# Performance work log

Hardware: AMD Instinct MI355X
Metric: run time of the kernel (lower is better)

## Reference

```python
import jax, jax.numpy as jnp
import numpy as np

SIGMA = 30.0
N, E = 50000, 1600000
IN_LOCAL, IN_GLOBAL, HIDDEN = 128, 128, 64


def setup_inputs() -> dict:
    key = jax.random.key(0)
    ks = jax.random.split(key, 20)
    inp = {}
    inp["x_local"] = jax.random.normal(ks[0], (N, IN_LOCAL), jnp.float32)
    inp["x_global"] = jax.random.normal(ks[1], (N, IN_GLOBAL), jnp.float32)
    inp["noise_features"] = jax.random.normal(ks[2], (N, 10), jnp.float32)
    inp["coord"] = jax.random.normal(ks[3], (N, 2), jnp.float32) * 30.0
    inp["edge_index"] = jax.random.randint(ks[4], (2, E), 0, N, jnp.int32)
    # EdgeWeightLayer params (torch init: eye fc1 weight, fixed fc2 weight, zero fc2 bias)
    inp["fc1_w"] = jnp.eye(10, dtype=jnp.float32)
    inp["fc1_b"] = jax.random.uniform(ks[5], (10,), jnp.float32, -0.3, 0.3)
    inp["fc2_w"] = jnp.array([[1.0, 0.7, 0.5, 0.3, -0.5, -0.8, -0.3, -0.5, 0.2, -0.2]], jnp.float32)
    inp["fc2_b"] = jnp.zeros((1,), jnp.float32)
    sl = 1.0 / np.sqrt(IN_LOCAL)
    inp["gat_w"] = jax.random.uniform(ks[6], (HIDDEN, IN_LOCAL), jnp.float32, -sl, sl)
    inp["gat_att_src"] = jax.random.uniform(ks[7], (HIDDEN,), jnp.float32, -sl, sl)
    inp["gat_att_dst"] = jax.random.uniform(ks[8], (HIDDEN,), jnp.float32, -sl, sl)
    inp["gat_b"] = jnp.zeros((HIDDEN,), jnp.float32)
    sg = 1.0 / np.sqrt(IN_GLOBAL)
    inp["gcn_w"] = jax.random.uniform(ks[9], (HIDDEN, IN_GLOBAL), jnp.float32, -sg, sg)
    inp["gcn_b"] = jnp.zeros((HIDDEN,), jnp.float32)
    sf = 1.0 / np.sqrt(2 * HIDDEN)
    inp["fus_w1"] = jax.random.uniform(ks[10], (HIDDEN, 2 * HIDDEN), jnp.float32, -sf, sf)
    inp["fus_b1"] = jax.random.uniform(ks[11], (HIDDEN,), jnp.float32, -sf, sf)
    sh = 1.0 / np.sqrt(HIDDEN)
    inp["fus_w2"] = jax.random.uniform(ks[12], (1, HIDDEN), jnp.float32, -sh, sh)
    inp["fus_b2"] = jax.random.uniform(ks[13], (1,), jnp.float32, -sh, sh)
    return inp


def _forward(edge_index, x_local, x_global, noise_features, coord,
             fc1_w, fc1_b, fc2_w, fc2_b,
             gat_w, gat_att_src, gat_att_dst, gat_b,
             gcn_w, gcn_b, fus_w1, fus_b1, fus_w2, fus_b2):
    n = x_local.shape[0]
    src, dst = edge_index[0], edge_index[1]

    # per-edge noise MLP on gathered source node features: [E,10]->[E]
    h = jax.nn.elu(noise_features[src] @ fc1_w.T + fc1_b)
    noise_ind = (h @ fc2_w.T + fc2_b)[:, 0]

    # gaussian distance kernel + smooth mapping into [0.1, 2.0]
    d2 = jnp.sum((coord[src] - coord[dst]) ** 2, axis=1)
    gw = jnp.exp(-d2 / (2.0 * SIGMA ** 2))
    w = 0.1 + 1.9 * jax.nn.sigmoid(gw * (1.0 + noise_ind) - 1.0)
    mask = w >= 0.2  # dynamic edge masking, expressed as weight masking (jit-safe)

    # append self loops (both GATConv and GCNConv add them by default)
    loop = jnp.arange(n, dtype=src.dtype)
    s_all = jnp.concatenate([src, loop])
    d_all = jnp.concatenate([dst, loop])
    m_all = jnp.concatenate([mask, jnp.ones((n,), bool)])

    # ---- GAT branch (1 head; PyG GATConv ignores scalar edge weight when edge_dim=None) ----
    xl = x_local @ gat_w.T                           # [N, H]
    a_src = xl @ gat_att_src                         # [N]
    a_dst = xl @ gat_att_dst
    e = jax.nn.leaky_relu(a_src[s_all] + a_dst[d_all], negative_slope=0.2)
    neg = jnp.finfo(e.dtype).min
    mx = jax.ops.segment_max(jnp.where(m_all, e, neg), d_all, num_segments=n)
    ex = jnp.where(m_all, jnp.exp(e - mx[d_all]), 0.0)
    den = jax.ops.segment_sum(ex, d_all, num_segments=n)
    alpha = ex / den[d_all]
    gat_out = jax.ops.segment_sum(alpha[:, None] * xl[s_all], d_all, num_segments=n) + gat_b
    x_l = jax.nn.elu(gat_out)

    # ---- GCN branch (symmetric norm with masked edge weights, self-loop weight 1) ----
    ew = jnp.concatenate([jnp.where(mask, w, 0.0), jnp.ones((n,), w.dtype)])
    deg = jax.ops.segment_sum(ew, d_all, num_segments=n)
    dis = jnp.where(deg > 0, jax.lax.rsqrt(deg), 0.0)
    norm = dis[s_all] * ew * dis[d_all]
    xg = x_global @ gcn_w.T                          # [N, H]
    gcn_out = jax.ops.segment_sum(norm[:, None] * xg[s_all], d_all, num_segments=n) + gcn_b
    x_g = jax.nn.relu(gcn_out)

    # ---- fusion head (dropout inactive at inference) ----
    cat = jnp.concatenate([x_l, x_g], axis=1)        # [N, 2H]
    hid = jax.nn.relu(cat @ fus_w1.T + fus_b1)
    out = hid @ fus_w2.T + fus_b2                    # [N, 1]
    return out[:, 0]


def reference(x_local, x_global, noise_features, coord, edge_index,
              fc1_w, fc1_b, fc2_w, fc2_b,
              gat_w, gat_att_src, gat_att_dst, gat_b,
              gcn_w, gcn_b, fus_w1, fus_b1, fus_w2, fus_b2):
    return _forward(edge_index, x_local, x_global, noise_features, coord,
                    fc1_w, fc1_b, fc2_w, fc2_b,
                    gat_w, gat_att_src, gat_att_dst, gat_b,
                    gcn_w, gcn_b, fus_w1, fus_b1, fus_w2, fus_b2)
```

## Files before the change

### kernel.cpp

```cpp
#include <hip/hip_runtime.h>
#include <hip/hip_fp16.h>
#include <math.h>

#define NN 50000
#define NE 1600000
#define NBIN 512
#define DSTF 98
#define NREP 8
#define PCAP 24
#define BCAPR 576

__device__ __forceinline__ float wave_sum(float v) {
    #pragma unroll
    for (int off = 32; off > 0; off >>= 1) v += __shfl_xor(v, off, 64);
    return v;
}

__global__ __launch_bounds__(256) void k_node_gat(
    const float* __restrict__ x_local, const float* __restrict__ gat_w,
    const float* __restrict__ att_src, const float* __restrict__ att_dst,
    const float* __restrict__ nf, const float* __restrict__ coord,
    const float* __restrict__ fc1_w, const float* __restrict__ fc1_b,
    const float* __restrict__ fc2_w, const float* __restrict__ fc2_b,
    __half* __restrict__ xch,
    float4* __restrict__ snode, float4* __restrict__ dnode,
    float* __restrict__ ps)
{
    __shared__ float wL[64 * 132];
    __shared__ float xt[32 * 128];
    for (int f = threadIdx.x; f < 64 * 128; f += 256) {
        int h = f >> 7, k = f & 127;
        wL[h * 132 + k] = gat_w[f];
    }
    const int lane = threadIdx.x & 63;
    const int wid  = threadIdx.x >> 6;
    const float asv = att_src[lane];
    const float adv = att_dst[lane];
    const float4* wrow = (const float4*)(wL + lane * 132);
    float4* xts = (float4*)xt;
    const float4* xp = (const float4*)x_local;
    for (int base = blockIdx.x * 32; base < NN; base += gridDim.x * 32) {
        __syncthreads();
        #pragma unroll
        for (int k = 0; k < 4; k++) {
            int gi = base * 32 + (int)threadIdx.x + k * 256;
            if (gi < NN * 32) xts[threadIdx.x + k * 256] = xp[gi];
        }
        __syncthreads();
        float acc[8] = {0.f,0.f,0.f,0.f,0.f,0.f,0.f,0.f};
        const float4* xrow = (const float4*)(xt + wid * 8 * 128);
        #pragma unroll 1
        for (int t = 0; t < 32; t++) {
            float4 wv = wrow[t];
            #pragma unroll
            for (int j = 0; j < 8; j++) {
                float4 xv = xrow[j * 32 + t];
                acc[j] = fmaf(xv.x, wv.x, acc[j]);
                acc[j] = fmaf(xv.y, wv.y, acc[j]);
                acc[j] = fmaf(xv.z, wv.z, acc[j]);
                acc[j] = fmaf(xv.w, wv.w, acc[j]);
            }
        }
        float sv[8], dv[8];
        #pragma unroll
        for (int j = 0; j < 8; j++) {
            int n = base + wid * 8 + j;
            if (n < NN) xch[(size_t)n * 128 + lane] = __float2half(acc[j]);
            sv[j] = wave_sum(acc[j] * asv);
            dv[j] = wave_sum(acc[j] * adv);
        }
        if (lane < 8) {
            int n = base + wid * 8 + lane;
            if (n < NN) {
                float svx = (lane==0)?sv[0]:(lane==1)?sv[1]:(lane==2)?sv[2]:(lane==3)?sv[3]
                           :(lane==4)?sv[4]:(lane==5)?sv[5]:(lane==6)?sv[6]:sv[7];
                float dvx = (lane==0)?dv[0]:(lane==1)?dv[1]:(lane==2)?dv[2]:(lane==3)?dv[3]
                           :(lane==4)?dv[4]:(lane==5)?dv[5]:(lane==6)?dv[6]:dv[7];
                float xvv[10];
                #pragma unroll
                for (int k = 0; k < 10; k++) xvv[k] = nf[n * 10 + k];
                float niv = fc2_b[0];
                #pragma unroll
                for (int j = 0; j < 10; j++) {
                    float h = fc1_b[j];
                    #pragma unroll
                    for (int k = 0; k < 10; k++) h = fmaf(xvv[k], fc1_w[j * 10 + k], h);
                    h = (h > 0.f) ? h : expm1f(h);
                    niv = fmaf(h, fc2_w[j], niv);
                }
                float cx = coord[2 * n], cy = coord[2 * n + 1];
                float es = svx + dvx;
                es = (es >= 0.f) ? es : 0.2f * es;
                snode[n] = make_float4(cx, cy, svx, niv);
                dnode[n] = make_float4(cx, cy, dvx, 0.f);
                ps[n] = __expf(es);
            }
        }
    }
}

__global__ __launch_bounds__(256) void k_node_gcn(
    const float* __restrict__ x_global, const float* __restrict__ gcn_w,
    __half* __restrict__ xch)
{
    __shared__ float wL[64 * 132];
    __shared__ float xt[32 * 128];
    for (int f = threadIdx.x; f < 64 * 128; f += 256) {
        int h = f >> 7, k = f & 127;
        wL[h * 132 + k] = gcn_w[f];
    }
    const int lane = threadIdx.x & 63;
    const int wid  = threadIdx.x >> 6;
    const float4* wrow = (const float4*)(wL + lane * 132);
    float4* xts = (float4*)xt;
    const float4* xp = (const float4*)x_global;
    for (int base = blockIdx.x * 32; base < NN; base += gridDim.x * 32) {
        __syncthreads();
        #pragma unroll
        for (int k = 0; k < 4; k++) {
            int gi = base * 32 + (int)threadIdx.x + k * 256;
            if (gi < NN * 32) xts[threadIdx.x + k * 256] = xp[gi];
        }
        __syncthreads();
        float acc[8] = {0.f,0.f,0.f,0.f,0.f,0.f,0.f,0.f};
        const float4* xrow = (const float4*)(xt + wid * 8 * 128);
        #pragma unroll 1
        for (int t = 0; t < 32; t++) {
            float4 wv = wrow[t];
            #pragma unroll
            for (int j = 0; j < 8; j++) {
                float4 xv = xrow[j * 32 + t];
                acc[j] = fmaf(xv.x, wv.x, acc[j]);
                acc[j] = fmaf(xv.y, wv.y, acc[j]);
                acc[j] = fmaf(xv.z, wv.z, acc[j]);
                acc[j] = fmaf(xv.w, wv.w, acc[j]);
            }
        }
        #pragma unroll
        for (int j = 0; j < 8; j++) {
            int n = base + wid * 8 + j;
            if (n < NN) xch[(size_t)n * 128 + 64 + lane] = __float2half(acc[j]);
        }
    }
}

__global__ __launch_bounds__(256) void k_zerog(unsigned int* __restrict__ gcnt)
{
    int i = blockIdx.x * 256 + threadIdx.x;
    if (i < NREP * NBIN) gcnt[i] = 0u;
}

__global__ __launch_bounds__(256) void k_part2(
    const int* __restrict__ ei,
    unsigned int* __restrict__ bucket, unsigned int* __restrict__ gcnt)
{
    __shared__ unsigned int lcnt[NBIN];
    __shared__ unsigned int lbase[NBIN];
    __shared__ unsigned int lbuf[NBIN][PCAP];
    const int rep = blockIdx.x & 7;
    for (int t = threadIdx.x; t < NBIN; t += 256) lcnt[t] = 0u;
    __syncthreads();
    const int base = blockIdx.x * 2048;
    #pragma unroll
    for (int k = 0; k < 8; k++) {
        int i = base + k * 256 + threadIdx.x;
        if (i < NE) {
            int d = ei[NE + i];
            int s = ei[i];
            int b = d / DSTF;
            unsigned int pk = (unsigned int)s | ((unsigned int)(d - b * DSTF) << 16);
            unsigned int slot = atomicAdd(&lcnt[b], 1u);
            if (slot < PCAP) {
                lbuf[b][slot] = pk;
            } else {
                unsigned int g = atomicAdd(&gcnt[rep * NBIN + b], 1u);
                if (g < BCAPR) bucket[(size_t)(rep * NBIN + b) * BCAPR + g] = pk;
            }
        }
    }
    __syncthreads();
    for (int t = threadIdx.x; t < NBIN; t += 256) {
        unsigned int n = lcnt[t];
        if (n > PCAP) n = PCAP;
        lcnt[t] = n;
        lbase[t] = n ? atomicAdd(&gcnt[rep * NBIN + t], n) : 0u;
    }
    __syncthreads();
    for (int t = threadIdx.x; t < NBIN; t += 256) {
        unsigned int n = lcnt[t];
        unsigned int gb = lbase[t];
        unsigned int* dst = bucket + (size_t)(rep * NBIN + t) * BCAPR;
        for (unsigned int e = 0; e < n; e++) {
            unsigned int g = gb + e;
            if (g < BCAPR) dst[g] = lbuf[t][e];
        }
    }
}

__global__ __launch_bounds__(512) void k_edge3(
    const unsigned int* __restrict__ bucket, const unsigned int* __restrict__ gcnt,
    const float4* __restrict__ snode, const float4* __restrict__ dnode,
    uint2* __restrict__ rec, unsigned int* __restrict__ offA,
    unsigned int* __restrict__ cntA, float* __restrict__ dis)
{
    const int bin = blockIdx.x;
    const int d0  = bin * DSTF;
    __shared__ unsigned int cnt[DSTF], off[DSTF], cur[DSTF], ews[DSTF];
    __shared__ float4 dnd[DSTF];
    __shared__ unsigned int segc[NREP];
    __shared__ unsigned int sm[128];
    __shared__ unsigned int wsum[8];
    __shared__ unsigned int sbase;
    for (int t = threadIdx.x; t < DSTF; t += 512) {
        cnt[t] = 0u; cur[t] = 0u; ews[t] = 0u;
        int d = d0 + t;
        dnd[t] = (d < NN) ? dnode[d] : make_float4(0.f, 0.f, 0.f, 0.f);
    }
    if (threadIdx.x < NREP) {
        unsigned int c = gcnt[threadIdx.x * NBIN + bin];
        segc[threadIdx.x] = (c > BCAPR) ? BCAPR : c;
    }
    unsigned int partial = 0u;
    for (int idx = threadIdx.x; idx < NREP * NBIN; idx += 512) {
        int b = idx & (NBIN - 1);
        if (b < bin) {
            unsigned int c = gcnt[(idx >> 9) * NBIN + b];
            partial += (c > BCAPR) ? BCAPR : c;
        }
    }
    #pragma unroll
    for (int o = 32; o > 0; o >>= 1) partial += __shfl_xor(partial, o, 64);
    if ((threadIdx.x & 63) == 0) wsum[threadIdx.x >> 6] = partial;
    __syncthreads();
    if (threadIdx.x == 0) {
        unsigned int a = 0;
        #pragma unroll
        for (int r = 0; r < 8; r++) a += wsum[r];
        sbase = a;
    }
    __syncthreads();
    #pragma unroll
    for (int r = 0; r < NREP; r++) {
        unsigned int c = segc[r];
        const unsigned int* bk = bucket + (size_t)(r * NBIN + bin) * BCAPR;
        for (unsigned int t = threadIdx.x; t < c; t += 512)
            atomicAdd(&cnt[bk[t] >> 16], 1u);
    }
    __syncthreads();
    if (threadIdx.x < 128) sm[threadIdx.x] = (threadIdx.x < DSTF) ? cnt[threadIdx.x] : 0u;
    __syncthreads();
    for (int o = 1; o < 128; o <<= 1) {
        unsigned int t = 0;
        if (threadIdx.x < 128 && threadIdx.x >= o) t = sm[threadIdx.x - o];
        __syncthreads();
        if (threadIdx.x < 128) sm[threadIdx.x] += t;
        __syncthreads();
    }
    if (threadIdx.x < DSTF) off[threadIdx.x] = sbase + sm[threadIdx.x] - cnt[threadIdx.x];
    __syncthreads();
    #pragma unroll
    for (int r = 0; r < NREP; r++) {
        unsigned int c = segc[r];
        const unsigned int* bk = bucket + (size_t)(r * NBIN + bin) * BCAPR;
        for (unsigned int t = threadIdx.x; t < c; t += 512) {
            unsigned int pk = bk[t];
            int dl = (int)(pk >> 16);
            int s  = (int)(pk & 0xFFFFu);
            float4 sv = snode[s];
            float4 dv = dnd[dl];
            float dx = sv.x - dv.x, dy = sv.y - dv.y;
            float gw = __expf((dx * dx + dy * dy) * (-1.0f / 1800.0f));
            float tt = fmaf(gw, 1.0f + sv.w, -1.0f);
            float sg = 1.0f / (1.0f + __expf(-tt));
            float w  = fmaf(1.9f, sg, 0.1f);
            float e  = sv.z + dv.z;
            e = (e >= 0.f) ? e : 0.2f * e;
            float ewv = (w >= 0.2f) ? w : 0.0f;
            float p = (ewv != 0.f) ? __expf(e) : 0.0f;
            unsigned int rk = atomicAdd(&cur[dl], 1u);
            atomicAdd(&ews[dl], (unsigned int)(ewv * 16777216.0f + 0.5f));
            __half2 h = __floats2half2_rn(p, ewv);
            rec[off[dl] + rk] = make_uint2((unsigned int)s, *(unsigned int*)&h);
        }
    }
    __syncthreads();
    for (int t = threadIdx.x; t < DSTF; t += 512) {
        int d = d0 + t;
        if (d < NN) {
            offA[d] = off[t];
            cntA[d] = cnt[t];
            dis[d]  = rsqrtf(1.0f + (float)ews[t] * (1.0f / 16777216.0f));
        }
    }
}

__global__ __launch_bounds__(256) void k_gather3(
    const __half* __restrict__ xch,
    const float* __restrict__ ps, const float* __restrict__ dis,
    const unsigned int* __restrict__ offA, const unsigned int* __restrict__ cntA,
    const uint2* __restrict__ rec,
    const float* __restrict__ gat_b, const float* __restrict__ gcn_b,
    uint2* __restrict__ catLh, uint2* __restrict__ catGh)
{
    const int lane = threadIdx.x & 63;
    const int wid  = threadIdx.x >> 6;
    const int eg   = lane >> 3;
    const int q    = lane & 7;
    const int fi   = q * 8;
    const float g0 = (eg == 0) ? 1.0f : 0.0f;
    const float4 gb0 = *(const float4*)(gat_b + fi);
    const float4 gb1 = *(const float4*)(gat_b + fi + 4);
    const float4 cb0 = *(const float4*)(gcn_b + fi);
    const float4 cb1 = *(const float4*)(gcn_b + fi + 4);
    for (int n = blockIdx.x * 4 + wid; n < NN; n += gridDim.x * 4) {
        float psv = ps[n] * g0;
        float dd = dis[n];
        int beg = (int)offA[n];
        int end = beg + (int)cntA[n];
        const uint4* rowd = (const uint4*)(xch + (size_t)n * 128);
        uint4 us = rowd[q];
        uint4 ug = rowd[q + 8];
        float2 d0 = __half22float2(*(const __half2*)&us.x);
        float2 d1 = __half22float2(*(const __half2*)&us.y);
        float2 d2 = __half22float2(*(const __half2*)&us.z);
        float2 d3 = __half22float2(*(const __half2*)&us.w);
        float2 e0 = __half22float2(*(const __half2*)&ug.x);
        float2 e1 = __half22float2(*(const __half2*)&ug.y);
        float2 e2 = __half22float2(*(const __half2*)&ug.z);
        float2 e3 = __half22float2(*(const __half2*)&ug.w);
        float aL[8], aC[8];
        aL[0] = psv * d0.x; aL[1] = psv * d0.y; aL[2] = psv * d1.x; aL[3] = psv * d1.y;
        aL[4] = psv * d2.x; aL[5] = psv * d2.y; aL[6] = psv * d3.x; aL[7] = psv * d3.y;
        float sw = dd * g0;
        aC[0] = sw * e0.x; aC[1] = sw * e0.y; aC[2] = sw * e1.x; aC[3] = sw * e1.y;
        aC[4] = sw * e2.x; aC[5] = sw * e2.y; aC[6] = sw * e3.x; aC[7] = sw * e3.y;
        float den = psv;
        int j = beg + eg;
        for (; j + 8 < end; j += 16) {
            uint2 r0 = rec[j];
            uint2 r1 = rec[j + 8];
            int s0 = (int)r0.x;
            int s1 = (int)r1.x;
            float2 pc0 = __half22float2(*(const __half2*)&r0.y);
            float2 pc1 = __half22float2(*(const __half2*)&r1.y);
            float c0 = dis[s0] * pc0.y;
            float c1 = dis[s1] * pc1.y;
            const uint4* row0 = (const uint4*)(xch + (size_t)s0 * 128);
            const uint4* row1 = (const uint4*)(xch + (size_t)s1 * 128);
            uint4 l0 = row0[q];
            uint4 g0v = row0[q + 8];
            uint4 l1 = row1[q];
            uint4 g1v = row1[q + 8];
            float2 t0, t1, t2, t3;
            t0 = __half22float2(*(const __half2*)&l0.x);
            t1 = __half22float2(*(const __half2*)&l0.y);
            t2 = __half22float2(*(const __half2*)&l0.z);
            t3 = __half22float2(*(const __half2*)&l0.w);
            aL[0] = fmaf(pc0.x, t0.x, aL[0]); aL[1] = fmaf(pc0.x, t0.y, aL[1]);
            aL[2] = fmaf(pc0.x, t1.x, aL[2]); aL[3] = fmaf(pc0.x, t1.y, aL[3]);
            aL[4] = fmaf(pc0.x, t2.x, aL[4]); aL[5] = fmaf(pc0.x, t2.y, aL[5]);
            aL[6] = fmaf(pc0.x, t3.x, aL[6]); aL[7] = fmaf(pc0.x, t3.y, aL[7]);
            t0 = __half22float2(*(const __half2*)&g0v.x);
            t1 = __half22float2(*(const __half2*)&g0v.y);
            t2 = __half22float2(*(const __half2*)&g0v.z);
            t3 = __half22float2(*(const __half2*)&g0v.w);
            aC[0] = fmaf(c0, t0.x, aC[0]); aC[1] = fmaf(c0, t0.y, aC[1]);
            aC[2] = fmaf(c0, t1.x, aC[2]); aC[3] = fmaf(c0, t1.y, aC[3]);
            aC[4] = fmaf(c0, t2.x, aC[4]); aC[5] = fmaf(c0, t2.y, aC[5]);
            aC[6] = fmaf(c0, t3.x, aC[6]); aC[7] = fmaf(c0, t3.y, aC[7]);
            t0 = __half22float2(*(const __half2*)&l1.x);
            t1 = __half22float2(*(const __half2*)&l1.y);
            t2 = __half22float2(*(const __half2*)&l1.z);
            t3 = __half22float2(*(const __half2*)&l1.w);
            aL[0] = fmaf(pc1.x, t0.x, aL[0]); aL[1] = fmaf(pc1.x, t0.y, aL[1]);
            aL[2] = fmaf(pc1.x, t1.x, aL[2]); aL[3] = fmaf(pc1.x, t1.y, aL[3]);
            aL[4] = fmaf(pc1.x, t2.x, aL[4]); aL[5] = fmaf(pc1.x, t2.y, aL[5]);
            aL[6] = fmaf(pc1.x, t3.x, aL[6]); aL[7] = fmaf(pc1.x, t3.y, aL[7]);
            t0 = __half22float2(*(const __half2*)&g1v.x);
            t1 = __half22float2(*(const __half2*)&g1v.y);
            t2 = __half22float2(*(const __half2*)&g1v.z);
            t3 = __half22float2(*(const __half2*)&g1v.w);
            aC[0] = fmaf(c1, t0.x, aC[0]); aC[1] = fmaf(c1, t0.y, aC[1]);
            aC[2] = fmaf(c1, t1.x, aC[2]); aC[3] = fmaf(c1, t1.y, aC[3]);
            aC[4] = fmaf(c1, t2.x, aC[4]); aC[5] = fmaf(c1, t2.y, aC[5]);
            aC[6] = fmaf(c1, t3.x, aC[6]); aC[7] = fmaf(c1, t3.y, aC[7]);
            den += pc0.x + pc1.x;
        }
        if (j < end) {
            uint2 r0 = rec[j];
            int s0 = (int)r0.x;
            float2 pc0 = __half22float2(*(const __half2*)&r0.y);
            float c0 = dis[s0] * pc0.y;
            const uint4* row0 = (const uint4*)(xch + (size_t)s0 * 128);
            uint4 l0 = row0[q];
            uint4 g0v = row0[q + 8];
            float2 t0, t1, t2, t3;
            t0 = __half22float2(*(const __half2*)&l0.x);
            t1 = __half22float2(*(const __half2*)&l0.y);
            t2 = __half22float2(*(const __half2*)&l0.z);
            t3 = __half22float2(*(const __half2*)&l0.w);
            aL[0] = fmaf(pc0.x, t0.x, aL[0]); aL[1] = fmaf(pc0.x, t0.y, aL[1]);
            aL[2] = fmaf(pc0.x, t1.x, aL[2]); aL[3] = fmaf(pc0.x, t1.y, aL[3]);
            aL[4] = fmaf(pc0.x, t2.x, aL[4]); aL[5] = fmaf(pc0.x, t2.y, aL[5]);
            aL[6] = fmaf(pc0.x, t3.x, aL[6]); aL[7] = fmaf(pc0.x, t3.y, aL[7]);
            t0 = __half22float2(*(const __half2*)&g0v.x);
            t1 = __half22float2(*(const __half2*)&g0v.y);
            t2 = __half22float2(*(const __half2*)&g0v.z);
            t3 = __half22float2(*(const __half2*)&g0v.w);
            aC[0] = fmaf(c0, t0.x, aC[0]); aC[1] = fmaf(c0, t0.y, aC[1]);
            aC[2] = fmaf(c0, t1.x, aC[2]); aC[3] = fmaf(c0, t1.y, aC[3]);
            aC[4] = fmaf(c0, t2.x, aC[4]); aC[5] = fmaf(c0, t2.y, aC[5]);
            aC[6] = fmaf(c0, t3.x, aC[6]); aC[7] = fmaf(c0, t3.y, aC[7]);
            den += pc0.x;
        }
        #pragma unroll
        for (int m = 8; m <= 32; m <<= 1) {
            #pragma unroll
            for (int k = 0; k < 8; k++) {
                aL[k] += __shfl_xor(aL[k], m, 64);
                aC[k] += __shfl_xor(aC[k], m, 64);
            }
            den += __shfl_xor(den, m, 64);
        }
        if (eg == 0) {
            float rd = 1.0f / den;
            float la[8], ga[8];
            la[0] = fmaf(aL[0], rd, gb0.x); la[1] = fmaf(aL[1], rd, gb0.y);
            la[2] = fmaf(aL[2], rd, gb0.z); la[3] = fmaf(aL[3], rd, gb0.w);
            la[4] = fmaf(aL[4], rd, gb1.x); la[5] = fmaf(aL[5], rd, gb1.y);
            la[6] = fmaf(aL[6], rd, gb1.z); la[7] = fmaf(aL[7], rd, gb1.w);
            ga[0] = fmaxf(fmaf(dd, aC[0], cb0.x), 0.f);
            ga[1] = fmaxf(fmaf(dd, aC[1], cb0.y), 0.f);
            ga[2] = fmaxf(fmaf(dd, aC[2], cb0.z), 0.f);
            ga[3] = fmaxf(fmaf(dd, aC[3], cb0.w), 0.f);
            ga[4] = fmaxf(fmaf(dd, aC[4], cb1.x), 0.f);
            ga[5] = fmaxf(fmaf(dd, aC[5], cb1.y), 0.f);
            ga[6] = fmaxf(fmaf(dd, aC[6], cb1.z), 0.f);
            ga[7] = fmaxf(fmaf(dd, aC[7], cb1.w), 0.f);
            #pragma unroll
            for (int k = 0; k < 8; k++)
                la[k] = (la[k] > 0.f) ? la[k] : expm1f(la[k]);
            __half2 l01 = __floats2half2_rn(la[0], la[1]);
            __half2 l23 = __floats2half2_rn(la[2], la[3]);
            __half2 l45 = __floats2half2_rn(la[4], la[5]);
            __half2 l67 = __floats2half2_rn(la[6], la[7]);
            __half2 g01 = __floats2half2_rn(ga[0], ga[1]);
            __half2 g23 = __floats2half2_rn(ga[2], ga[3]);
            __half2 g45 = __floats2half2_rn(ga[4], ga[5]);
            __half2 g67 = __floats2half2_rn(ga[6], ga[7]);
            catLh[(size_t)n * 16 + q * 2] =
                make_uint2(*(unsigned int*)&l01, *(unsigned int*)&l23);
            catLh[(size_t)n * 16 + q * 2 + 1] =
                make_uint2(*(unsigned int*)&l45, *(unsigned int*)&l67);
            catGh[(size_t)n * 16 + q * 2] =
                make_uint2(*(unsigned int*)&g01, *(unsigned int*)&g23);
            catGh[(size_t)n * 16 + q * 2 + 1] =
                make_uint2(*(unsigned int*)&g45, *(unsigned int*)&g67);
        }
    }
}

__global__ __launch_bounds__(256) void k_fuse(
    const uint2* __restrict__ catLh, const uint2* __restrict__ catGh,
    const float* __restrict__ fus_w1, const float* __restrict__ fus_b1,
    const float* __restrict__ fus_w2, const float* __restrict__ fus_b2,
    float* __restrict__ out)
{
    __shared__ float wS[64 * 132];
    __shared__ uint2 catS[32 * 33];
    const int nb = blockIdx.x * 32;
    for (int f = threadIdx.x; f < 64 * 128; f += 256) {
        int r = f >> 7, c = f & 127;
        wS[r * 132 + c] = fus_w1[f];
    }
    for (int f = threadIdx.x; f < 32 * 32; f += 256) {
        int i = f >> 5, c = f & 31;
        int n = nb + i;
        uint2 v = make_uint2(0u, 0u);
        if (n < NN) v = (c < 16) ? catLh[(size_t)n * 16 + c]
                                 : catGh[(size_t)n * 16 + (c - 16)];
        catS[i * 33 + c] = v;
    }
    __syncthreads();
    const int p = threadIdx.x >> 3;
    const int q = threadIdx.x & 7;
    const int n = nb + p;
    float hid[8];
    #pragma unroll
    for (int j = 0; j < 8; j++) {
        int jj = (q + j) & 7;
        hid[j] = fus_b1[q * 8 + jj];
    }
    const uint2* cp = catS + p * 33;
    #pragma unroll 2
    for (int kb = 0; kb < 32; kb++) {
        uint2 u = cp[kb];
        float2 a = __half22float2(*(const __half2*)&u.x);
        float2 b = __half22float2(*(const __half2*)&u.y);
        #pragma unroll
        for (int j = 0; j < 8; j++) {
            int jj = (q + j) & 7;
            float4 wv = *(const float4*)(wS + (size_t)(q * 8 + jj) * 132 + kb * 4);
            hid[j] = fmaf(wv.x, a.x, hid[j]);
            hid[j] = fmaf(wv.y, a.y, hid[j]);
            hid[j] = fmaf(wv.z, b.x, hid[j]);
            hid[j] = fmaf(wv.w, b.y, hid[j]);
        }
    }
    float acc = 0.f;
    #pragma unroll
    for (int j = 0; j < 8; j++) {
        int jj = (q + j) & 7;
        acc = fmaf(fmaxf(hid[j], 0.f), fus_w2[q * 8 + jj], acc);
    }
    acc += __shfl_xor(acc, 1, 64);
    acc += __shfl_xor(acc, 2, 64);
    acc += __shfl_xor(acc, 4, 64);
    if (q == 0 && n < NN) out[n] = acc + fus_b2[0];
}

extern "C" void kernel_launch(void* const* d_in, const int* in_sizes, int n_in,
                              void* d_out, int out_size, void* d_ws, size_t ws_size,
                              hipStream_t stream)
{
    const float* x_local  = (const float*)d_in[0];
    const float* x_global = (const float*)d_in[1];
    const float* nf       = (const float*)d_in[2];
    const float* coord    = (const float*)d_in[3];
    const int*   ei       = (const int*)d_in[4];
    const float* fc1_w    = (const float*)d_in[5];
    const float* fc1_b    = (const float*)d_in[6];
    const float* fc2_w    = (const float*)d_in[7];
    const float* fc2_b    = (const float*)d_in[8];
    const float* gat_w    = (const float*)d_in[9];
    const float* att_src  = (const float*)d_in[10];
    const float* att_dst  = (const float*)d_in[11];
    const float* gat_b    = (const float*)d_in[12];
    const float* gcn_w    = (const float*)d_in[13];
    const float* gcn_b    = (const float*)d_in[14];
    const float* fus_w1   = (const float*)d_in[15];
    const float* fus_b1   = (const float*)d_in[16];
    const float* fus_w2   = (const float*)d_in[17];
    const float* fus_b2   = (const float*)d_in[18];
    float* out = (float*)d_out;

    char* ws = (char*)d_ws;
    uint2*  rec  = (uint2*) (ws);
    __half* xch  = (__half*)(ws + 12800000);
    uint2*  catLh= (uint2*) (ws + 25600000);
    uint2*  catGh= (uint2*) (ws + 32000000);
    unsigned int* bucket = (unsigned int*)(ws + 25600000);
    float4* snode= (float4*)(ws + 38400000);
    float4* dnode= (float4*)(ws + 39200000);
    unsigned int* offA = (unsigned int*)(ws + 40000000);
    unsigned int* cntA = (unsigned int*)(ws + 40200000);
    float*  dis  = (float*) (ws + 40400000);
    float*  ps   = (float*) (ws + 40600000);
    unsigned int* gcnt = (unsigned int*)(ws + 40800000);
    (void)in_sizes; (void)n_in; (void)out_size; (void)ws_size;

    k_zerog<<<(NREP * NBIN + 255) / 256, 256, 0, stream>>>(gcnt);
    k_part2<<<782, 256, 0, stream>>>(ei, bucket, gcnt);
    k_node_gat<<<782, 256, 0, stream>>>(x_local, gat_w, att_src, att_dst,
                                        nf, coord, fc1_w, fc1_b, fc2_w, fc2_b,
                                        xch, snode, dnode, ps);
    k_node_gcn<<<782, 256, 0, stream>>>(x_global, gcn_w, xch);
    k_edge3<<<NBIN, 512, 0, stream>>>(bucket, gcnt, snode, dnode,
                                      rec, offA, cntA, dis);
    k_gather3<<<3125, 256, 0, stream>>>(xch, ps, dis, offA, cntA, rec,
                                        gat_b, gcn_b, catLh, catGh);
    k_fuse<<<(NN + 31) / 32, 256, 0, stream>>>(catLh, catGh,
                                               fus_w1, fus_b1, fus_w2, fus_b2, out);
}
```

Measured before the change: 323.0 us.

## Merge edge partition and both node projection kernels into one launch

Combines the edge bucketing kernel and the GAT and GCN node projection kernels into a single kernel whose blocks are split by block index into three roles. Each role keeps its original logic and reuses one shared-memory buffer sized for the largest role. The goal is to remove two kernel launches and the idle tail between them, letting the independent stages run concurrently on the GPU. In exchange every block reserves the largest shared-memory footprint, which can lower occupancy for the projection blocks.

```diff
diff --git a/kernel.cpp b/kernel.cpp
--- a/kernel.cpp
+++ b/kernel.cpp
@@ -9,6 +9,7 @@
 #define NREP 8
 #define PCAP 24
 #define BCAPR 576
+#define NBF 782
 
 __device__ __forceinline__ float wave_sum(float v) {
     #pragma unroll
@@ -16,183 +17,150 @@
     return v;
 }
 
-__global__ __launch_bounds__(256) void k_node_gat(
+__global__ __launch_bounds__(256) void k_zerog(unsigned int* __restrict__ gcnt)
+{
+    int i = blockIdx.x * 256 + threadIdx.x;
+    if (i < NREP * NBIN) gcnt[i] = 0u;
+}
+
+__global__ __launch_bounds__(256) void k_front(
+    const int* __restrict__ ei,
+    unsigned int* __restrict__ bucket, unsigned int* __restrict__ gcnt,
     const float* __restrict__ x_local, const float* __restrict__ gat_w,
     const float* __restrict__ att_src, const float* __restrict__ att_dst,
     const float* __restrict__ nf, const float* __restrict__ coord,
     const float* __restrict__ fc1_w, const float* __restrict__ fc1_b,
     const float* __restrict__ fc2_w, const float* __restrict__ fc2_b,
+    const float* __restrict__ x_global, const float* __restrict__ gcn_w,
     __half* __restrict__ xch,
     float4* __restrict__ snode, float4* __restrict__ dnode,
     float* __restrict__ ps)
 {
-    __shared__ float wL[64 * 132];
-    __shared__ float xt[32 * 128];
-    for (int f = threadIdx.x; f < 64 * 128; f += 256) {
-        int h = f >> 7, k = f & 127;
-        wL[h * 132 + k] = gat_w[f];
-    }
-    const int lane = threadIdx.x & 63;
-    const int wid  = threadIdx.x >> 6;
-    const float asv = att_src[lane];
-    const float adv = att_dst[lane];
-    const float4* wrow = (const float4*)(wL + lane * 132);
-    float4* xts = (float4*)xt;
-    const float4* xp = (const float4*)x_local;
-    for (int base = blockIdx.x * 32; base < NN; base += gridDim.x * 32) {
+    __shared__ unsigned int smem[13312];
+    const int bid = blockIdx.x;
+    if (bid < NBF) {
+        unsigned int* lcnt  = smem;
+        unsigned int* lbase = smem + NBIN;
+        unsigned int (*lbuf)[PCAP] = (unsigned int(*)[PCAP])(smem + 2 * NBIN);
+        const int rep = bid & 7;
+        for (int t = threadIdx.x; t < NBIN; t += 256) lcnt[t] = 0u;
         __syncthreads();
+        const int base = bid * 2048;
         #pragma unroll
-        for (int k = 0; k < 4; k++) {
-            int gi = base * 32 + (int)threadIdx.x + k * 256;
-            if (gi < NN * 32) xts[threadIdx.x + k * 256] = xp[gi];
+        for (int k = 0; k < 8; k++) {
+            int i = base + k * 256 + threadIdx.x;
+            if (i < NE) {
+                int d = ei[NE + i];
+                int s = ei[i];
+                int b = d / DSTF;
+                unsigned int pk = (unsigned int)s | ((unsigned int)(d - b * DSTF) << 16);
+                unsigned int slot = atomicAdd(&lcnt[b], 1u);
+                if (slot < PCAP) {
+                    lbuf[b][slot] = pk;
+                } else {
+                    unsigned int g = atomicAdd(&gcnt[rep * NBIN + b], 1u);
+                    if (g < BCAPR) bucket[(size_t)(rep * NBIN + b) * BCAPR + g] = pk;
+                }
+            }
         }
         __syncthreads();
-        float acc[8] = {0.f,0.f,0.f,0.f,0.f,0.f,0.f,0.f};
-        const float4* xrow = (const float4*)(xt + wid * 8 * 128);
-        #pragma unroll 1
-        for (int t = 0; t < 32; t++) {
-            float4 wv = wrow[t];
+        for (int t = threadIdx.x; t < NBIN; t += 256) {
+            unsigned int n = lcnt[t];
+            if (n > PCAP) n = PCAP;
+            lcnt[t] = n;
+            lbase[t] = n ? atomicAdd(&gcnt[rep * NBIN + t], n) : 0u;
+        }
+        __syncthreads();
+        for (int t = threadIdx.x; t < NBIN; t += 256) {
+            unsigned int n = lcnt[t];
+            unsigned int gb = lbase[t];
+            unsigned int* dst = bucket + (size_t)(rep * NBIN + t) * BCAPR;
+            for (unsigned int e = 0; e < n; e++) {
+                unsigned int g = gb + e;
+                if (g < BCAPR) dst[g] = lbuf[t][e];
+            }
+        }
+    } else {
+        const bool isGat = bid < 2 * NBF;
+        const int vb = isGat ? bid - NBF : bid - 2 * NBF;
+        const float* xsrc = isGat ? x_local : x_global;
+        const float* wsrc = isGat ? gat_w : gcn_w;
+        float* wL = (float*)smem;
+        float* xt = (float*)smem + 64 * 132;
+        for (int f = threadIdx.x; f < 64 * 128; f += 256) {
+            int h = f >> 7, k = f & 127;
+            wL[h * 132 + k] = wsrc[f];
+        }
+        const int lane = threadIdx.x & 63;
+        const int wid  = threadIdx.x >> 6;
+        const float asv = att_src[lane];
+        const float adv = att_dst[lane];
+        const int ofs = isGat ? 0 : 64;
+        const float4* wrow = (const float4*)(wL + lane * 132);
+        float4* xts = (float4*)xt;
+        const float4* xp = (const float4*)xsrc;
+        for (int base = vb * 32; base < NN; base += NBF * 32) {
+            __syncthreads();
+            #pragma unroll
+            for (int k = 0; k < 4; k++) {
+                int gi = base * 32 + (int)threadIdx.x + k * 256;
+                if (gi < NN * 32) xts[threadIdx.x + k * 256] = xp[gi];
+            }
+            __syncthreads();
+            float acc[8] = {0.f,0.f,0.f,0.f,0.f,0.f,0.f,0.f};
+            const float4* xrow = (const float4*)(xt + wid * 8 * 128);
+            #pragma unroll 1
+            for (int t = 0; t < 32; t++) {
+                float4 wv = wrow[t];
+                #pragma unroll
+                for (int j = 0; j < 8; j++) {
+                    float4 xv = xrow[j * 32 + t];
+                    acc[j] = fmaf(xv.x, wv.x, acc[j]);
+                    acc[j] = fmaf(xv.y, wv.y, acc[j]);
+                    acc[j] = fmaf(xv.z, wv.z, acc[j]);
+                    acc[j] = fmaf(xv.w, wv.w, acc[j]);
+                }
+            }
             #pragma unroll
             for (int j = 0; j < 8; j++) {
-                float4 xv = xrow[j * 32 + t];
-                acc[j] = fmaf(xv.x, wv.x, acc[j]);
-                acc[j] = fmaf(xv.y, wv.y, acc[j]);
-                acc[j] = fmaf(xv.z, wv.z, acc[j]);
-                acc[j] = fmaf(xv.w, wv.w, acc[j]);
-            }
-        }
-        float sv[8], dv[8];
-        #pragma unroll
-        for (int j = 0; j < 8; j++) {
-            int n = base + wid * 8 + j;
-            if (n < NN) xch[(size_t)n * 128 + lane] = __float2half(acc[j]);
-            sv[j] = wave_sum(acc[j] * asv);
-            dv[j] = wave_sum(acc[j] * adv);
-        }
-        if (lane < 8) {
-            int n = base + wid * 8 + lane;
-            if (n < NN) {
-                float svx = (lane==0)?sv[0]:(lane==1)?sv[1]:(lane==2)?sv[2]:(lane==3)?sv[3]
-                           :(lane==4)?sv[4]:(lane==5)?sv[5]:(lane==6)?sv[6]:sv[7];
-                float dvx = (lane==0)?dv[0]:(lane==1)?dv[1]:(lane==2)?dv[2]:(lane==3)?dv[3]
-                           :(lane==4)?dv[4]:(lane==5)?dv[5]:(lane==6)?dv[6]:dv[7];
-                float xvv[10];
+                int n = base + wid * 8 + j;
+                if (n < NN) xch[(size_t)n * 128 + ofs + lane] = __float2half(acc[j]);
+            }
+            if (isGat) {
+                float sv[8], dv[8];
                 #pragma unroll
-                for (int k = 0; k < 10; k++) xvv[k] = nf[n * 10 + k];
-                float niv = fc2_b[0];
-                #pragma unroll
-                for (int j = 0; j < 10; j++) {
-                    float h = fc1_b[j];
-                    #pragma unroll
-                    for (int k = 0; k < 10; k++) h = fmaf(xvv[k], fc1_w[j * 10 + k], h);
-                    h = (h > 0.f) ? h : expm1f(h);
-                    niv = fmaf(h, fc2_w[j], niv);
+                for (int j = 0; j < 8; j++) {
+                    sv[j] = wave_sum(acc[j] * asv);
+                    dv[j] = wave_sum(acc[j] * adv);
                 }
-                float cx = coord[2 * n], cy = coord[2 * n + 1];
-                float es = svx + dvx;
-                es = (es >= 0.f) ? es : 0.2f * es;
-                snode[n] = make_float4(cx, cy, svx, niv);
-                dnode[n] = make_float4(cx, cy, dvx, 0.f);
-                ps[n] = __expf(es);
-            }
-        }
-    }
-}
-
-__global__ __launch_bounds__(256) void k_node_gcn(
-    const float* __restrict__ x_global, const float* __restrict__ gcn_w,
-    __half* __restrict__ xch)
-{
-    __shared__ float wL[64 * 132];
-    __shared__ float xt[32 * 128];
-    for (int f = threadIdx.x; f < 64 * 128; f += 256) {
-        int h = f >> 7, k = f & 127;
-        wL[h * 132 + k] = gcn_w[f];
-    }
-    const int lane = threadIdx.x & 63;
-    const int wid  = threadIdx.x >> 6;
-    const float4* wrow = (const float4*)(wL + lane * 132);
-    float4* xts = (float4*)xt;
-    const float4* xp = (const float4*)x_global;
-    for (int base = blockIdx.x * 32; base < NN; base += gridDim.x * 32) {
-        __syncthreads();
-        #pragma unroll
-        for (int k = 0; k < 4; k++) {
-            int gi = base * 32 + (int)threadIdx.x + k * 256;
-            if (gi < NN * 32) xts[threadIdx.x + k * 256] = xp[gi];
-        }
-        __syncthreads();
-        float acc[8] = {0.f,0.f,0.f,0.f,0.f,0.f,0.f,0.f};
-        const float4* xrow = (const float4*)(xt + wid * 8 * 128);
-        #pragma unroll 1
-        for (int t = 0; t < 32; t++) {
-            float4 wv = wrow[t];
-            #pragma unroll
-            for (int j = 0; j < 8; j++) {
-                float4 xv = xrow[j * 32 + t];
-                acc[j] = fmaf(xv.x, wv.x, acc[j]);
-                acc[j] = fmaf(xv.y, wv.y, acc[j]);
-                acc[j] = fmaf(xv.z, wv.z, acc[j]);
-                acc[j] = fmaf(xv.w, wv.w, acc[j]);
-            }
-        }
-        #pragma unroll
-        for (int j = 0; j < 8; j++) {
-            int n = base + wid * 8 + j;
-            if (n < NN) xch[(size_t)n * 128 + 64 + lane] = __float2half(acc[j]);
-        }
-    }
-}
-
-__global__ __launch_bounds__(256) void k_zerog(unsigned int* __restrict__ gcnt)
-{
-    int i = blockIdx.x * 256 + threadIdx.x;
-    if (i < NREP * NBIN) gcnt[i] = 0u;
-}
-
-__global__ __launch_bounds__(256) void k_part2(
-    const int* __restrict__ ei,
-    unsigned int* __restrict__ bucket, unsigned int* __restrict__ gcnt)
-{
-    __shared__ unsigned int lcnt[NBIN];
-    __shared__ unsigned int lbase[NBIN];
-    __shared__ unsigned int lbuf[NBIN][PCAP];
-    const int rep = blockIdx.x & 7;
-    for (int t = threadIdx.x; t < NBIN; t += 256) lcnt[t] = 0u;
-    __syncthreads();
-    const int base = blockIdx.x * 2048;
-    #pragma unroll
-    for (int k = 0; k < 8; k++) {
-        int i = base + k * 256 + threadIdx.x;
-        if (i < NE) {
-            int d = ei[NE + i];
-            int s = ei[i];
-            int b = d / DSTF;
-            unsigned int pk = (unsigned int)s | ((unsigned int)(d - b * DSTF) << 16);
-            unsigned int slot = atomicAdd(&lcnt[b], 1u);
-            if (slot < PCAP) {
-                lbuf[b][slot] = pk;
-            } else {
-                unsigned int g = atomicAdd(&gcnt[rep * NBIN + b], 1u);
-                if (g < BCAPR) bucket[(size_t)(rep * NBIN + b) * BCAPR + g] = pk;
-            }
-        }
-    }
-    __syncthreads();
-    for (int t = threadIdx.x; t < NBIN; t += 256) {
-        unsigned int n = lcnt[t];
-        if (n > PCAP) n = PCAP;
-        lcnt[t] = n;
-        lbase[t] = n ? atomicAdd(&gcnt[rep * NBIN + t], n) : 0u;
-    }
-    __syncthreads();
-    for (int t = threadIdx.x; t < NBIN; t += 256) {
-        unsigned int n = lcnt[t];
-        unsigned int gb = lbase[t];
-        unsigned int* dst = bucket + (size_t)(rep * NBIN + t) * BCAPR;
-        for (unsigned int e = 0; e < n; e++) {
-            unsigned int g = gb + e;
-            if (g < BCAPR) dst[g] = lbuf[t][e];
+                if (lane < 8) {
+                    int n = base + wid * 8 + lane;
+                    if (n < NN) {
+                        float svx = (lane==0)?sv[0]:(lane==1)?sv[1]:(lane==2)?sv[2]:(lane==3)?sv[3]
+                                   :(lane==4)?sv[4]:(lane==5)?sv[5]:(lane==6)?sv[6]:sv[7];
+                        float dvx = (lane==0)?dv[0]:(lane==1)?dv[1]:(lane==2)?dv[2]:(lane==3)?dv[3]
+                                   :(lane==4)?dv[4]:(lane==5)?dv[5]:(lane==6)?dv[6]:dv[7];
+                        float xvv[10];
+                        #pragma unroll
+                        for (int k = 0; k < 10; k++) xvv[k] = nf[n * 10 + k];
+                        float niv = fc2_b[0];
+                        #pragma unroll
+                        for (int j = 0; j < 10; j++) {
+                            float h = fc1_b[j];
+                            #pragma unroll
+                            for (int k = 0; k < 10; k++) h = fmaf(xvv[k], fc1_w[j * 10 + k], h);
+                            h = (h > 0.f) ? h : expm1f(h);
+                            niv = fmaf(h, fc2_w[j], niv);
+                        }
+                        float cx = coord[2 * n], cy = coord[2 * n + 1];
+                        float es = svx + dvx;
+                        es = (es >= 0.f) ? es : 0.2f * es;
+                        snode[n] = make_float4(cx, cy, svx, niv);
+                        dnode[n] = make_float4(cx, cy, dvx, 0.f);
+                        ps[n] = __expf(es);
+                    }
+                }
+            }
         }
     }
 }
@@ -560,11 +528,11 @@
     (void)in_sizes; (void)n_in; (void)out_size; (void)ws_size;
 
     k_zerog<<<(NREP * NBIN + 255) / 256, 256, 0, stream>>>(gcnt);
-    k_part2<<<782, 256, 0, stream>>>(ei, bucket, gcnt);
-    k_node_gat<<<782, 256, 0, stream>>>(x_local, gat_w, att_src, att_dst,
-                                        nf, coord, fc1_w, fc1_b, fc2_w, fc2_b,
-                                        xch, snode, dnode, ps);
-    k_node_gcn<<<782, 256, 0, stream>>>(x_global, gcn_w, xch);
+    k_front<<<3 * NBF, 256, 0, stream>>>(ei, bucket, gcnt,
+                                         x_local, gat_w, att_src, att_dst,
+                                         nf, coord, fc1_w, fc1_b, fc2_w, fc2_b,
+                                         x_global, gcn_w,
+                                         xch, snode, dnode, ps);
     k_edge3<<<NBIN, 512, 0, stream>>>(bucket, gcnt, snode, dnode,
                                       rec, offA, cntA, dis);
     k_gather3<<<3125, 256, 0, stream>>>(xch, ps, dis, offA, cntA, rec,
```

Result: faster. 286.1 us (-11.4%).
